# Optimization experiments

Hardware: AMD Instinct MI355X
Metric: run time of the kernel (lower is better)

Reference implementation:

```python
import jax, jax.numpy as jnp
import numpy as np

N_FEAT = 1024
NEG_BIG = -1e30  # finite stand-in for -inf to avoid NaNs on fully-masked rows


def setup_inputs() -> dict:
    key = jax.random.key(0)
    k1, k2, k3 = jax.random.split(key, 3)
    T, C = 4096, 1024
    x = jax.random.normal(k1, (T, C), dtype=jnp.float32)
    W = jax.random.normal(k2, (C, 3 * N_FEAT), dtype=jnp.float32) * 0.02
    b = jax.random.normal(k3, (3 * N_FEAT,), dtype=jnp.float32) * 0.02
    return {"x": x, "W": W, "b": b, "n_padd": 256}


def reference(x, W, b, n_padd):
    T, C = x.shape
    qkv = x @ W + b  # [T, 3*N_FEAT]
    q, k, v = jnp.split(qkv, 3, axis=1)  # each [T, N_FEAT]
    att = (q @ k.T) * (1.0 / jnp.sqrt(jnp.float32(N_FEAT)))  # [T, T]
    idx = jnp.arange(T)
    causal = idx[None, :] <= idx[:, None]
    data = (idx[None, :] >= n_padd) & (idx[:, None] >= n_padd)
    mask = causal & data
    att = jnp.where(mask, att, NEG_BIG)
    p = jax.nn.softmax(att, axis=-1)  # fully-masked rows -> uniform, zeroed below
    y = p @ v  # [T, N_FEAT]
    # kernel only stores rows >= n_padd; padded rows defined as zero here
    y = jnp.where(idx[:, None] >= n_padd, y, 0.0)
    return y
```

## Files before the change

kernel.cpp:

```cpp
#include <hip/hip_runtime.h>
#include <hip/hip_bf16.h>
#include <stdint.h>
#include <stddef.h>

#define TT 4096
#define CC 1024
#define NFD 1024
#define N3 3072
#define JSPLIT 17

typedef __bf16 bf16;
typedef __bf16 bf16x8 __attribute__((ext_vector_type(8)));
typedef __bf16 bf16x4 __attribute__((ext_vector_type(4)));
typedef float f32x4 __attribute__((ext_vector_type(4)));

typedef const __attribute__((address_space(1))) unsigned char gl_u8;
typedef __attribute__((address_space(3))) unsigned char lds_u8;

__device__ __forceinline__ void glds16(const void* g, void* l) {
  __builtin_amdgcn_global_load_lds((gl_u8*)g, (lds_u8*)l, 16, 0, 0);
}

__device__ __forceinline__ void stage128x32(const bf16* __restrict__ src, int ld, bf16* lds, int tid) {
  const int lane = tid & 63;
  const int w = tid >> 6;
#pragma unroll
  for (int p = 0; p < 2; ++p) {
    const int lbyte = w * 2048 + p * 1024;
    const int row = (lbyte >> 6) + (lane >> 2);
    const int kel = (lane & 3) << 3;
    glds16(src + row * ld + kel, (char*)lds + lbyte);
  }
}

__device__ __forceinline__ void gemm_core(const bf16* __restrict__ A, const bf16* __restrict__ B,
                                          int lda, int ldb, int ksteps,
                                          bf16* As, bf16* Bs, int tid, f32x4 (&acc)[4][4]) {
  const int lane = tid & 63;
  const int w = tid >> 6;
  const int wm = (w >> 1) * 64;
  const int wn = (w & 1) * 64;
  const int lrow = lane & 15;
  const int lko = (lane >> 4) * 8;
  stage128x32(A, lda, As, tid);
  stage128x32(B, ldb, Bs, tid);
  __syncthreads();
  for (int ks = 0; ks < ksteps; ++ks) {
    const bf16* Ac = As + (ks & 1) * 4096;
    const bf16* Bc = Bs + (ks & 1) * 4096;
    if (ks + 1 < ksteps) {
      stage128x32(A + (ks + 1) * 32, lda, As + ((ks + 1) & 1) * 4096, tid);
      stage128x32(B + (ks + 1) * 32, ldb, Bs + ((ks + 1) & 1) * 4096, tid);
    }
    bf16x8 af[4], bfr[4];
#pragma unroll
    for (int i = 0; i < 4; ++i)
      af[i] = *(const bf16x8*)(Ac + (wm + i * 16 + lrow) * 32 + lko);
#pragma unroll
    for (int i = 0; i < 4; ++i)
      bfr[i] = *(const bf16x8*)(Bc + (wn + i * 16 + lrow) * 32 + lko);
#pragma unroll
    for (int mi = 0; mi < 4; ++mi)
#pragma unroll
      for (int ni = 0; ni < 4; ++ni)
        acc[mi][ni] = __builtin_amdgcn_mfma_f32_16x16x32_bf16(af[mi], bfr[ni], acc[mi][ni], 0, 0, 0);
    __syncthreads();
  }
}

__global__ __launch_bounds__(256) void k_prep(const float* __restrict__ x, bf16* __restrict__ xb,
                                              const float* __restrict__ Wsrc, bf16* __restrict__ WbT) {
  __shared__ float Ls[64][68];
  const int tid = threadIdx.x;
  if (blockIdx.x < 2048) {
    int idx = (blockIdx.x * 256 + tid) * 8;
    f32x4 a = *(const f32x4*)(x + idx);
    f32x4 b = *(const f32x4*)(x + idx + 4);
    bf16x8 o;
#pragma unroll
    for (int j = 0; j < 4; ++j) { o[j] = (bf16)a[j]; o[4 + j] = (bf16)b[j]; }
    *(bf16x8*)(xb + idx) = o;
    return;
  }
  const int bid = blockIdx.x - 2048;
  const int n0 = (bid % 48) * 64;
  const int c0 = (bid / 48) * 64;
#pragma unroll
  for (int qq = 0; qq < 4; ++qq) {
    int lin = qq * 1024 + tid * 4;
    int r = lin >> 6, cc = lin & 63;
    f32x4 v = *(const f32x4*)(Wsrc + (size_t)(c0 + r) * N3 + n0 + cc);
#pragma unroll
    for (int j = 0; j < 4; ++j) Ls[r][cc + j] = v[j];
  }
  __syncthreads();
#pragma unroll
  for (int qq = 0; qq < 4; ++qq) {
    int lin = qq * 1024 + tid * 4;
    int nr = lin >> 6, cc = lin & 63;
    bf16x4 o;
#pragma unroll
    for (int j = 0; j < 4; ++j) o[j] = (bf16)Ls[cc + j][nr];
    *(bf16x4*)(WbT + (size_t)(n0 + nr) * CC + c0 + cc) = o;
  }
}

__global__ __launch_bounds__(256, 2) void k_qkv(const bf16* __restrict__ xb, const bf16* __restrict__ wbt,
                                                const float* __restrict__ bias,
                                                bf16* __restrict__ q, bf16* __restrict__ k,
                                                bf16* __restrict__ vT) {
  __shared__ bf16 As[2 * 128 * 32], Bs[2 * 128 * 32];
  const int tid = threadIdx.x;
  const int m0 = blockIdx.y * 128;
  const int n0 = blockIdx.x * 128;
  f32x4 acc[4][4];
#pragma unroll
  for (int i = 0; i < 4; ++i)
#pragma unroll
    for (int j = 0; j < 4; ++j) acc[i][j] = (f32x4){0.f, 0.f, 0.f, 0.f};

  gemm_core(xb + (size_t)m0 * CC, wbt + (size_t)n0 * CC, CC, CC, CC / 32, As, Bs, tid, acc);

  const int lane = tid & 63;
  const int w = tid >> 6;
  const int wm = (w >> 1) * 64, wn = (w & 1) * 64;
  const int seg = n0 >> 10;
#pragma unroll
  for (int mi = 0; mi < 4; ++mi) {
    const int tB = m0 + wm + mi * 16 + ((lane >> 4) << 2);
#pragma unroll
    for (int ni = 0; ni < 4; ++ni) {
      const int n = n0 + wn + ni * 16 + (lane & 15);
      const float bb = bias[n];
      f32x4 a = acc[mi][ni];
      if (seg == 2) {
        bf16x4 pv;
#pragma unroll
        for (int r = 0; r < 4; ++r) pv[r] = (bf16)(a[r] + bb);
        *(bf16x4*)(vT + (size_t)(n - 2048) * TT + tB) = pv;
      } else {
        bf16* dst = (seg == 0) ? q : k;
        const int nl = n & 1023;
#pragma unroll
        for (int r = 0; r < 4; ++r) dst[(size_t)(tB + r) * NFD + nl] = (bf16)(a[r] + bb);
      }
    }
  }
}

__global__ __launch_bounds__(256, 2) void k_scores(const bf16* __restrict__ q, const bf16* __restrict__ kk,
                                                   bf16* __restrict__ P, float* __restrict__ l,
                                                   const int* __restrict__ npadd_p) {
  const int jt = blockIdx.x, it = blockIdx.y;
  const int np = *npadd_p;
  const int jt0 = np >> 7;
  if (jt > it || jt < jt0) return;
  __shared__ bf16 As[2 * 128 * 32], Bs[2 * 128 * 32];
  const int tid = threadIdx.x;
  f32x4 acc[4][4];
#pragma unroll
  for (int i = 0; i < 4; ++i)
#pragma unroll
    for (int j = 0; j < 4; ++j) acc[i][j] = (f32x4){0.f, 0.f, 0.f, 0.f};

  gemm_core(q + (size_t)it * 128 * CC, kk + (size_t)jt * 128 * CC, CC, CC, CC / 32, As, Bs, tid, acc);

  const int lane = tid & 63;
  const int w = tid >> 6;
  const int wm = (w >> 1) * 64, wn = (w & 1) * 64;
  const float scale = 0.03125f;
#pragma unroll
  for (int mi = 0; mi < 4; ++mi) {
    const int iB = it * 128 + wm + mi * 16 + ((lane >> 4) << 2);
    float rs[4] = {0.f, 0.f, 0.f, 0.f};
#pragma unroll
    for (int ni = 0; ni < 4; ++ni) {
      const int j = jt * 128 + wn + ni * 16 + (lane & 15);
      f32x4 a = acc[mi][ni];
#pragma unroll
      for (int r = 0; r < 4; ++r) {
        const int i = iB + r;
        float p = 0.f;
        if (j <= i && j >= np && i >= np) p = __expf(a[r] * scale);
        const bf16 pb = (bf16)p;
        P[(size_t)i * TT + j] = pb;
        rs[r] += (float)pb;
      }
    }
#pragma unroll
    for (int r = 0; r < 4; ++r) {
      float v = rs[r];
      v += __shfl_xor(v, 1);
      v += __shfl_xor(v, 2);
      v += __shfl_xor(v, 4);
      v += __shfl_xor(v, 8);
      if ((lane & 15) == 0) atomicAdd(&l[iB + r], v);
    }
  }
}

__global__ __launch_bounds__(256, 2) void k_pvc(const bf16* __restrict__ P, const bf16* __restrict__ vT,
                                                bf16* __restrict__ part0, bf16* __restrict__ part1,
                                                const int* __restrict__ npadd_p) {
  const int c = blockIdx.x;
  const int it = blockIdx.y;
  const int d0 = blockIdx.z * 128;
  const int np = *npadd_p;
  const int jt0 = np >> 7;
  int jlo, jhi;
  if (c == 0) { jlo = jt0;                      jhi = min(JSPLIT, it + 1); }
  else        { jlo = max(JSPLIT, jt0);         jhi = it + 1; }
  if (jlo >= jhi) return;

  __shared__ bf16 As[2 * 128 * 32], Bs[2 * 128 * 32];
  const int tid = threadIdx.x;
  f32x4 acc[4][4];
#pragma unroll
  for (int i = 0; i < 4; ++i)
#pragma unroll
    for (int j = 0; j < 4; ++j) acc[i][j] = (f32x4){0.f, 0.f, 0.f, 0.f};

  gemm_core(P + (size_t)it * 128 * TT + (size_t)jlo * 128,
            vT + (size_t)d0 * TT + (size_t)jlo * 128,
            TT, TT, (jhi - jlo) * 4, As, Bs, tid, acc);

  bf16* __restrict__ part = (c == 0) ? part0 : part1;
  const int lane = tid & 63;
  const int w = tid >> 6;
  const int wm = (w >> 1) * 64, wn = (w & 1) * 64;
#pragma unroll
  for (int mi = 0; mi < 4; ++mi) {
    const int iB = it * 128 + wm + mi * 16 + ((lane >> 4) << 2);
#pragma unroll
    for (int ni = 0; ni < 4; ++ni) {
      const int d = d0 + wn + ni * 16 + (lane & 15);
      f32x4 a = acc[mi][ni];
#pragma unroll
      for (int r = 0; r < 4; ++r)
        part[(size_t)(iB + r) * NFD + d] = (bf16)a[r];
    }
  }
}

__global__ __launch_bounds__(256) void k_norm(const bf16* __restrict__ part0, const bf16* __restrict__ part1,
                                              const float* __restrict__ l, float* __restrict__ y,
                                              const int* __restrict__ npadd_p) {
  const int idx = (blockIdx.x * 256 + threadIdx.x) * 8;
  const int i = idx >> 10;
  const int np = *npadd_p;
  const int jt0 = np >> 7;
  const int it = i >> 7;
  float s[8] = {0.f, 0.f, 0.f, 0.f, 0.f, 0.f, 0.f, 0.f};
  float inv = 0.f;
  if (i >= np) {
    inv = 1.0f / l[i];
    if (min(JSPLIT, it + 1) > jt0) {
      bf16x8 a = *(const bf16x8*)(part0 + idx);
#pragma unroll
      for (int j = 0; j < 8; ++j) s[j] += (float)a[j];
    }
    if (it + 1 > max(JSPLIT, jt0)) {
      bf16x8 b = *(const bf16x8*)(part1 + idx);
#pragma unroll
      for (int j = 0; j < 8; ++j) s[j] += (float)b[j];
    }
  }
  f32x4 o0, o1;
#pragma unroll
  for (int j = 0; j < 4; ++j) { o0[j] = s[j] * inv; o1[j] = s[4 + j] * inv; }
  *(f32x4*)(y + idx) = o0;
  *(f32x4*)(y + idx + 4) = o1;
}

extern "C" void kernel_launch(void* const* d_in, const int* in_sizes, int n_in,
                              void* d_out, int out_size, void* d_ws, size_t ws_size,
                              hipStream_t stream) {
  const float* x = (const float*)d_in[0];
  const float* W = (const float*)d_in[1];
  const float* b = (const float*)d_in[2];
  const int* npadd = (const int*)d_in[3];
  float* y = (float*)d_out;

  char* ws = (char*)d_ws;
  const size_t MB = 1u << 20;
  bf16* q  = (bf16*)(ws + 0 * MB);
  bf16* kk = (bf16*)(ws + 8 * MB);
  bf16* part0 = (bf16*)(ws + 0 * MB);
  bf16* part1 = (bf16*)(ws + 8 * MB);
  bf16* vT = (bf16*)(ws + 16 * MB);
  float* l = (float*)(ws + 24 * MB);
  bf16* P  = (bf16*)(ws + 24 * MB + 65536);
  bf16* xb = P;
  bf16* WbT = (bf16*)((char*)P + 8 * MB);

  k_prep<<<dim3(2048 + 768), 256, 0, stream>>>(x, xb, W, WbT);
  k_qkv<<<dim3(N3 / 128, TT / 128), 256, 0, stream>>>(xb, WbT, b, q, kk, vT);
  hipMemsetAsync(l, 0, TT * sizeof(float), stream);
  k_scores<<<dim3(TT / 128, TT / 128), 256, 0, stream>>>(q, kk, P, l, npadd);
  k_pvc<<<dim3(2, TT / 128, NFD / 128), 256, 0, stream>>>(P, vT, part0, part1, npadd);
  k_norm<<<dim3((TT * NFD) / (256 * 8)), 256, 0, stream>>>(part0, part1, l, y, npadd);
}
```

Baseline: 132.9 us.

## Remap scores grid to causal tiles and fuse normalization into PV epilogue

The scores kernel now launches only the 528 lower-triangular 128x128 tiles instead of a full 32x32 grid. A banded, XCD-strided index mapping turns each block id into its (it, jt) tile. When only one split partition covers a row tile, the PV kernel scales by 1/l and writes fp32 output directly, so those rows skip the bf16 partial round-trip through the norm kernel. The norm kernel now only zeroes padded rows and combines the two partials for rows that actually have both. This cuts empty block launches and global memory traffic, at the cost of more complex index arithmetic.

Measured after the change: 128.5 us. 3.3% less time.

```diff
diff --git a/kernel.cpp b/kernel.cpp
--- a/kernel.cpp
+++ b/kernel.cpp
@@ -151,10 +151,29 @@
 __global__ __launch_bounds__(256, 2) void k_scores(const bf16* __restrict__ q, const bf16* __restrict__ kk,
                                                    bf16* __restrict__ P, float* __restrict__ l,
                                                    const int* __restrict__ npadd_p) {
-  const int jt = blockIdx.x, it = blockIdx.y;
+  const int id = blockIdx.x;
+  const int lin = (id & 7) * 66 + (id >> 3);
+  int band, rem;
+  if (lin < 228)      { band = 0; rem = lin; }
+  else if (lin < 392) { band = 1; rem = lin - 228; }
+  else if (lin < 492) { band = 2; rem = lin - 392; }
+  else                { band = 3; rem = lin - 492; }
+  int it, jt;
+  if (rem < 28) {
+    int itp = (int)((sqrtf(8.0f * (float)rem + 1.0f) - 1.0f) * 0.5f);
+    while ((itp + 1) * (itp + 2) / 2 <= rem) ++itp;
+    while (itp * (itp + 1) / 2 > rem) --itp;
+    it = band * 8 + itp;
+    jt = band * 8 + (rem - itp * (itp + 1) / 2);
+  } else {
+    const int rem2 = rem - 28;
+    it = band * 8 + 7 + (rem2 >> 3);
+    jt = band * 8 + (rem2 & 7);
+  }
   const int np = *npadd_p;
   const int jt0 = np >> 7;
-  if (jt > it || jt < jt0) return;
+  if (jt < jt0) return;
+
   __shared__ bf16 As[2 * 128 * 32], Bs[2 * 128 * 32];
   const int tid = threadIdx.x;
   f32x4 acc[4][4];
@@ -201,6 +220,7 @@
 
 __global__ __launch_bounds__(256, 2) void k_pvc(const bf16* __restrict__ P, const bf16* __restrict__ vT,
                                                 bf16* __restrict__ part0, bf16* __restrict__ part1,
+                                                const float* __restrict__ l, float* __restrict__ y,
                                                 const int* __restrict__ npadd_p) {
   const int c = blockIdx.x;
   const int it = blockIdx.y;
@@ -208,8 +228,8 @@
   const int np = *npadd_p;
   const int jt0 = np >> 7;
   int jlo, jhi;
-  if (c == 0) { jlo = jt0;                      jhi = min(JSPLIT, it + 1); }
-  else        { jlo = max(JSPLIT, jt0);         jhi = it + 1; }
+  if (c == 0) { jlo = jt0;              jhi = min(JSPLIT, it + 1); }
+  else        { jlo = max(JSPLIT, jt0); jhi = it + 1; }
   if (jlo >= jhi) return;
 
   __shared__ bf16 As[2 * 128 * 32], Bs[2 * 128 * 32];
@@ -224,20 +244,42 @@
             vT + (size_t)d0 * TT + (size_t)jlo * 128,
             TT, TT, (jhi - jlo) * 4, As, Bs, tid, acc);
 
-  bf16* __restrict__ part = (c == 0) ? part0 : part1;
   const int lane = tid & 63;
   const int w = tid >> 6;
   const int wm = (w >> 1) * 64, wn = (w & 1) * 64;
-#pragma unroll
-  for (int mi = 0; mi < 4; ++mi) {
-    const int iB = it * 128 + wm + mi * 16 + ((lane >> 4) << 2);
-#pragma unroll
-    for (int ni = 0; ni < 4; ++ni) {
-      const int d = d0 + wn + ni * 16 + (lane & 15);
-      f32x4 a = acc[mi][ni];
-#pragma unroll
-      for (int r = 0; r < 4; ++r)
-        part[(size_t)(iB + r) * NFD + d] = (bf16)a[r];
+  const bool sole = (c == 0) ? (jhi == it + 1) : (jlo == jt0);
+  if (sole) {
+#pragma unroll
+    for (int mi = 0; mi < 4; ++mi) {
+      const int iB = it * 128 + wm + mi * 16 + ((lane >> 4) << 2);
+      float inv4[4];
+#pragma unroll
+      for (int r = 0; r < 4; ++r) {
+        const int i = iB + r;
+        inv4[r] = (i >= np) ? (1.0f / l[i]) : 0.0f;
+      }
+#pragma unroll
+      for (int ni = 0; ni < 4; ++ni) {
+        const int d = d0 + wn + ni * 16 + (lane & 15);
+        f32x4 a = acc[mi][ni];
+#pragma unroll
+        for (int r = 0; r < 4; ++r)
+          y[(size_t)(iB + r) * NFD + d] = a[r] * inv4[r];
+      }
+    }
+  } else {
+    bf16* __restrict__ part = (c == 0) ? part0 : part1;
+#pragma unroll
+    for (int mi = 0; mi < 4; ++mi) {
+      const int iB = it * 128 + wm + mi * 16 + ((lane >> 4) << 2);
+#pragma unroll
+      for (int ni = 0; ni < 4; ++ni) {
+        const int d = d0 + wn + ni * 16 + (lane & 15);
+        f32x4 a = acc[mi][ni];
+#pragma unroll
+        for (int r = 0; r < 4; ++r)
+          part[(size_t)(iB + r) * NFD + d] = (bf16)a[r];
+      }
     }
   }
 }
@@ -250,24 +292,22 @@
   const int np = *npadd_p;
   const int jt0 = np >> 7;
   const int it = i >> 7;
-  float s[8] = {0.f, 0.f, 0.f, 0.f, 0.f, 0.f, 0.f, 0.f};
-  float inv = 0.f;
-  if (i >= np) {
-    inv = 1.0f / l[i];
-    if (min(JSPLIT, it + 1) > jt0) {
-      bf16x8 a = *(const bf16x8*)(part0 + idx);
-#pragma unroll
-      for (int j = 0; j < 8; ++j) s[j] += (float)a[j];
-    }
-    if (it + 1 > max(JSPLIT, jt0)) {
-      bf16x8 b = *(const bf16x8*)(part1 + idx);
-#pragma unroll
-      for (int j = 0; j < 8; ++j) s[j] += (float)b[j];
-    }
-  }
+  if (i < np) {
+    f32x4 z = (f32x4){0.f, 0.f, 0.f, 0.f};
+    *(f32x4*)(y + idx) = z;
+    *(f32x4*)(y + idx + 4) = z;
+    return;
+  }
+  if ((it + 1 <= JSPLIT) || (jt0 >= JSPLIT)) return;
+  const float inv = 1.0f / l[i];
+  bf16x8 a = *(const bf16x8*)(part0 + idx);
+  bf16x8 b = *(const bf16x8*)(part1 + idx);
   f32x4 o0, o1;
 #pragma unroll
-  for (int j = 0; j < 4; ++j) { o0[j] = s[j] * inv; o1[j] = s[4 + j] * inv; }
+  for (int j = 0; j < 4; ++j) {
+    o0[j] = ((float)a[j] + (float)b[j]) * inv;
+    o1[j] = ((float)a[4 + j] + (float)b[4 + j]) * inv;
+  }
   *(f32x4*)(y + idx) = o0;
   *(f32x4*)(y + idx + 4) = o1;
 }
@@ -296,7 +336,7 @@
   k_prep<<<dim3(2048 + 768), 256, 0, stream>>>(x, xb, W, WbT);
   k_qkv<<<dim3(N3 / 128, TT / 128), 256, 0, stream>>>(xb, WbT, b, q, kk, vT);
   hipMemsetAsync(l, 0, TT * sizeof(float), stream);
-  k_scores<<<dim3(TT / 128, TT / 128), 256, 0, stream>>>(q, kk, P, l, npadd);
-  k_pvc<<<dim3(2, TT / 128, NFD / 128), 256, 0, stream>>>(P, vT, part0, part1, npadd);
+  k_scores<<<dim3(528), 256, 0, stream>>>(q, kk, P, l, npadd);
+  k_pvc<<<dim3(2, TT / 128, NFD / 128), 256, 0, stream>>>(P, vT, part0, part1, l, y, npadd);
   k_norm<<<dim3((TT * NFD) / (256 * 8)), 256, 0, stream>>>(part0, part1, l, y, npadd);
 }
```
